# Optimization experiments

Hardware: AMD Instinct MI355X
Metric: run time of the kernel (lower is better)

The kernel has to match this reference:

```python
import jax, jax.numpy as jnp
import numpy as np

NEG_SLOPE_GAT = 0.2   # GATConv internal leaky_relu slope (PyG default)
NEG_SLOPE = 0.01      # nn.LeakyReLU default slope


def _gat(h_src_in, h_dst_in, src, dst, Wsrc, Wdst, a_s, a_d, b, n_dst, self_loops):
    """Single-head PyG-style GATConv: gather -> score -> edge softmax -> scatter-sum."""
    hs = h_src_in @ Wsrc            # [N_src, C]
    hd = h_dst_in @ Wdst            # [N_dst, C]
    if self_loops:                  # static flag; same node set on both sides
        loop = jnp.arange(n_dst, dtype=src.dtype)
        src = jnp.concatenate([src, loop])
        dst = jnp.concatenate([dst, loop])
    # attention logits per edge
    e = jax.nn.leaky_relu((hs @ a_s)[src] + (hd @ a_d)[dst], NEG_SLOPE_GAT)  # [E]
    # softmax over edges sharing a destination node
    m = jax.ops.segment_max(e, dst, num_segments=n_dst)
    ex = jnp.exp(e - m[dst])
    denom = jax.ops.segment_sum(ex, dst, num_segments=n_dst)
    alpha = ex / denom[dst]
    out = jax.ops.segment_sum(hs[src] * alpha[:, None], dst, num_segments=n_dst)
    return out + b


def setup_inputs() -> dict:
    key = jax.random.key(0)
    ks = iter(jax.random.split(key, 64))
    NB, NP = 100_000, 50_000
    E_bb, E_pp, E_bp = 800_000, 400_000, 400_000
    FB, FP, H, H2 = 32, 34, 64, 32
    rn = lambda shape, s=0.05: jax.random.normal(next(ks), shape, jnp.float32) * s
    d = {}
    d['x_b'] = rn((NB, FB), 1.0)
    d['x_p'] = rn((NP, FP), 1.0)
    d['ei_bb'] = jax.random.randint(next(ks), (2, E_bb), 0, NB, jnp.int32)
    d['ei_pp'] = jax.random.randint(next(ks), (2, E_pp), 0, NP, jnp.int32)
    d['ei_bp_src'] = jax.random.randint(next(ks), (E_bp,), 0, NB, jnp.int32)
    d['ei_bp_dst'] = jax.random.randint(next(ks), (E_bp,), 0, NP, jnp.int32)
    d['W_in_b'] = rn((FB, H)); d['b_in_b'] = jnp.zeros((H,), jnp.float32)
    d['W_in_p'] = rn((FP, H)); d['b_in_p'] = jnp.zeros((H,), jnp.float32)
    for tag, cin, cout in (('1', H, H), ('2', H, H2)):
        d['W_bb' + tag] = rn((cin, cout)); d['as_bb' + tag] = rn((cout,)); d['ad_bb' + tag] = rn((cout,)); d['b_bb' + tag] = jnp.zeros((cout,), jnp.float32)
        d['W_pp' + tag] = rn((cin, cout)); d['as_pp' + tag] = rn((cout,)); d['ad_pp' + tag] = rn((cout,)); d['b_pp' + tag] = jnp.zeros((cout,), jnp.float32)
        d['Ws_bp' + tag] = rn((cin, cout)); d['Wd_bp' + tag] = rn((cin, cout)); d['as_bp' + tag] = rn((cout,)); d['ad_bp' + tag] = rn((cout,)); d['b_bp' + tag] = jnp.zeros((cout,), jnp.float32)
    d['W_out'] = rn((H2, 1)); d['b_out'] = jnp.zeros((1,), jnp.float32)
    return d


def reference(x_b, x_p, ei_bb, ei_pp, ei_bp_src, ei_bp_dst,
              W_in_b, b_in_b, W_in_p, b_in_p,
              W_bb1, as_bb1, ad_bb1, b_bb1, W_pp1, as_pp1, ad_pp1, b_pp1,
              Ws_bp1, Wd_bp1, as_bp1, ad_bp1, b_bp1,
              W_bb2, as_bb2, ad_bb2, b_bb2, W_pp2, as_pp2, ad_pp2, b_pp2,
              Ws_bp2, Wd_bp2, as_bp2, ad_bp2, b_bp2,
              W_out, b_out):
    NB, NP = x_b.shape[0], x_p.shape[0]
    lr = lambda v: jax.nn.leaky_relu(v, NEG_SLOPE)
    # input projections (dropout is eval-mode identity)
    hb = lr(x_b @ W_in_b + b_in_b)
    hp = lr(x_p @ W_in_p + b_in_p)
    # hetero conv 1 (sum aggregation over relations sharing a dst type)
    ob = _gat(hb, hb, ei_bb[0], ei_bb[1], W_bb1, W_bb1, as_bb1, ad_bb1, b_bb1, NB, True)
    op = (_gat(hp, hp, ei_pp[0], ei_pp[1], W_pp1, W_pp1, as_pp1, ad_pp1, b_pp1, NP, True)
          + _gat(hb, hp, ei_bp_src, ei_bp_dst, Ws_bp1, Wd_bp1, as_bp1, ad_bp1, b_bp1, NP, False))
    hb, hp = lr(ob), lr(op)
    # hetero conv 2
    ob2 = _gat(hb, hb, ei_bb[0], ei_bb[1], W_bb2, W_bb2, as_bb2, ad_bb2, b_bb2, NB, True)
    op2 = (_gat(hp, hp, ei_pp[0], ei_pp[1], W_pp2, W_pp2, as_pp2, ad_pp2, b_pp2, NP, True)
           + _gat(hb, hp, ei_bp_src, ei_bp_dst, Ws_bp2, Wd_bp2, as_bp2, ad_bp2, b_bp2, NP, False))
    hp = lr(op2)
    return hp @ W_out + b_out  # [NP, 1]
```

## Files before the change

### kernel.cpp

```cpp
#include <hip/hip_runtime.h>
#include <hip/hip_bf16.h>
#include <cstdint>
#include <cstddef>


typedef __attribute__((ext_vector_type(8))) short short8;
typedef __attribute__((ext_vector_type(4))) float f32x4;
typedef unsigned int u32;
typedef __hip_bfloat16 bf16;

#define ABITS 9
#define CHUNKE 8192

static __device__ __forceinline__ float b2f(bf16 v) { return __bfloat162float(v); }

static __device__ __forceinline__ float ldf(const void* p, int i, int bf) {
    return bf ? __bfloat162float(((const bf16*)p)[i]) : ((const float*)p)[i];
}

static __device__ __forceinline__ short f2bs(float f) {
    bf16 h = __float2bfloat16(f);
    return *reinterpret_cast<short*>(&h);
}
static __device__ __forceinline__ float bs2f(short s) {
    bf16 h = *reinterpret_cast<bf16*>(&s);
    return __bfloat162float(h);
}
static __device__ __forceinline__ float lo16(u32 u) { return bs2f((short)(u & 0xffffu)); }
static __device__ __forceinline__ float hi16(u32 u) { return bs2f((short)(u >> 16)); }
static __device__ __forceinline__ u32 pack2(float x, float y) {
    return (u32)(unsigned short)f2bs(x) | ((u32)(unsigned short)f2bs(y) << 16);
}
static __device__ __forceinline__ float sel4(const float* a, int i) {
    return i == 0 ? a[0] : i == 1 ? a[1] : i == 2 ? a[2] : a[3];
}
static __device__ __forceinline__ float lrelu2(float x) { return x > 0.f ? x : 0.2f * x; }

static __device__ __forceinline__ int probe_bf(const unsigned* __restrict__ w, int* cnt) {
    if (threadIdx.x == 0) *cnt = 0;
    __syncthreads();
    int c = 0;
#pragma unroll
    for (int j = 0; j < 4; ++j) {
        unsigned u = w[threadIdx.x * 4 + j];
        unsigned e = (u >> 7) & 0xffu;
        c += (e >= 100u && e <= 145u) ? 1 : 0;
    }
    atomicAdd(cnt, c);
    __syncthreads();
    int r = (*cnt > 614) ? 1 : 0;
    __syncthreads();
    return r;
}

template <int CIN>
static __device__ __forceinline__ void in_proj_body(
    short* WT, float* bl, int bid,
    const void* __restrict__ X, const void* __restrict__ W, const void* __restrict__ B,
    bf16* __restrict__ Y, int M, int bf)
{
    constexpr int KP = 40;
    for (int i = threadIdx.x; i < 64 * CIN; i += 256) {
        int n = i / CIN, k = i - n * CIN;
        WT[n * KP + k] = f2bs(ldf(W, k * 64 + n, bf));
    }
    if (threadIdx.x < 64) bl[threadIdx.x] = ldf(B, threadIdx.x, bf);
    __syncthreads();

    int lane = threadIdx.x & 63;
    int wv   = threadIdx.x >> 6;
    int m = lane & 15, quad = lane >> 4;
    int row0 = (bid * 4 + wv) * 16;
    if (row0 >= M) return;

    int arow = row0 + m; if (arow >= M) arow = M - 1;
    short8 a;
#pragma unroll
    for (int j = 0; j < 8; ++j)
        a[j] = f2bs(ldf(X, arow * CIN + quad * 8 + j, bf));

    f32x4 acc[4] = {};
#pragma unroll
    for (int tt = 0; tt < 4; ++tt) {
        short8 bfr = *(const short8*)&WT[((lane & 15) + 16 * tt) * KP + quad * 8];
        acc[tt] = __builtin_amdgcn_mfma_f32_16x16x32_bf16(a, bfr, acc[tt], 0, 0, 0);
    }

    if (CIN == 34) {
        float x32[4], x33[4];
#pragma unroll
        for (int r = 0; r < 4; ++r) {
            int row = row0 + quad * 4 + r; if (row >= M) row = M - 1;
            x32[r] = ldf(X, row * CIN + 32, bf);
            x33[r] = ldf(X, row * CIN + 33, bf);
        }
#pragma unroll
        for (int tt = 0; tt < 4; ++tt) {
            int col = (lane & 15) + 16 * tt;
            float w32 = bs2f(WT[col * KP + 32]);
            float w33 = bs2f(WT[col * KP + 33]);
#pragma unroll
            for (int r = 0; r < 4; ++r)
                acc[tt][r] += x32[r] * w32 + x33[r] * w33;
        }
    }

#pragma unroll
    for (int tt = 0; tt < 4; ++tt) {
        int col = (lane & 15) + 16 * tt;
        float bb = bl[col];
#pragma unroll
        for (int r = 0; r < 4; ++r) {
            int row = row0 + quad * 4 + r;
            if (row < M) {
                float v = acc[tt][r] + bb;
                v = v > 0.f ? v : 0.01f * v;
                Y[(size_t)row * 64 + col] = __float2bfloat16(v);
            }
        }
    }
}

__global__ __launch_bounds__(256) void k_hist_inproj(
    const int* __restrict__ bb_d, const int* __restrict__ pp_d,
    const int* __restrict__ bp_d, int* __restrict__ histM,
    const unsigned* __restrict__ probe_w, int* __restrict__ flag,
    int E_bb, int E_pp, int E_bp, int NB, int NP, int nbkt, int nblk,
    const void* __restrict__ Xb, const void* __restrict__ Wb, const void* __restrict__ Bb,
    bf16* __restrict__ Yb, int MB,
    const void* __restrict__ Xp, const void* __restrict__ Wp, const void* __restrict__ Bp,
    bf16* __restrict__ Yp, int MP)
{
    __shared__ short WT[64 * 40];
    __shared__ float bl[64];
    __shared__ int aux[1 << ABITS];
    if ((int)blockIdx.x < nblk) {
        if (blockIdx.x == 0) {
            int b = probe_bf(probe_w, &aux[0]);
            if (threadIdx.x == 0) *flag = b;
        }
        for (int i = threadIdx.x; i < nbkt; i += 256) aux[i] = 0;
        __syncthreads();
        int E_all = E_bb + E_pp + E_bp;
        int base = blockIdx.x * CHUNKE;
        int end = base + CHUNKE < E_all ? base + CHUNKE : E_all;
        for (int i = base + threadIdx.x; i < end; i += 256) {
            int d;
            if (i < E_bb) d = bb_d[i];
            else if (i < E_bb + E_pp) d = NB + pp_d[i - E_bb];
            else d = NB + NP + bp_d[i - E_bb - E_pp];
            atomicAdd(&aux[d >> ABITS], 1);
        }
        __syncthreads();
        for (int i = threadIdx.x; i < nbkt; i += 256)
            histM[(size_t)i * nblk + blockIdx.x] = aux[i];
    } else {
        int bfv = probe_bf(probe_w, &aux[0]);
        int bid = blockIdx.x - nblk;
        int nbb = (MB + 63) >> 6;
        if (bid < nbb) in_proj_body<32>(WT, bl, bid, Xb, Wb, Bb, Yb, MB, bfv);
        else           in_proj_body<34>(WT, bl, bid - nbb, Xp, Wp, Bp, Yp, MP, bfv);
    }
}

__global__ __launch_bounds__(1024) void k_scan1(const int* __restrict__ deg,
                                                int* __restrict__ out,
                                                int* __restrict__ bsum, int n)
{
    __shared__ int wsum[16];
    int gid = blockIdx.x * 1024 + threadIdx.x;
    int lane = threadIdx.x & 63, wid = threadIdx.x >> 6;
    int v = (gid < n) ? deg[gid] : 0;
    int x = v;
#pragma unroll
    for (int off = 1; off < 64; off <<= 1) {
        int y = __shfl_up(x, off, 64);
        if (lane >= off) x += y;
    }
    if (lane == 63) wsum[wid] = x;
    __syncthreads();
    if (wid == 0 && lane < 16) {
        int w0 = wsum[lane];
#pragma unroll
        for (int off = 1; off < 16; off <<= 1) {
            int y = __shfl_up(w0, off, 16);
            if (lane >= off) w0 += y;
        }
        wsum[lane] = w0;
    }
    __syncthreads();
    int base = (wid > 0) ? wsum[wid - 1] : 0;
    int incl = base + x;
    if (gid < n) out[gid] = incl - v;
    if (threadIdx.x == 1023) bsum[blockIdx.x] = incl;
}

__global__ __launch_bounds__(1024) void k_scan2(int* __restrict__ bsum, int nb)
{
    __shared__ int wsum[16];
    int lane = threadIdx.x & 63, wid = threadIdx.x >> 6;
    int v = (threadIdx.x < nb) ? bsum[threadIdx.x] : 0;
    int x = v;
#pragma unroll
    for (int off = 1; off < 64; off <<= 1) {
        int y = __shfl_up(x, off, 64);
        if (lane >= off) x += y;
    }
    if (lane == 63) wsum[wid] = x;
    __syncthreads();
    if (wid == 0 && lane < 16) {
        int w0 = wsum[lane];
#pragma unroll
        for (int off = 1; off < 16; off <<= 1) {
            int y = __shfl_up(w0, off, 16);
            if (lane >= off) w0 += y;
        }
        wsum[lane] = w0;
    }
    __syncthreads();
    int base = (wid > 0) ? wsum[wid - 1] : 0;
    if (threadIdx.x < nb) bsum[threadIdx.x] = base + x - v;
}

__global__ __launch_bounds__(1024) void k_scan3(int* __restrict__ indptr,
                                                const int* __restrict__ bsum,
                                                int n, int E)
{
    int gid = blockIdx.x * 1024 + threadIdx.x;
    if (gid < n) indptr[gid] += bsum[blockIdx.x];
    if (gid == 0) indptr[n] = E;
}

template <int N1, int N2, bool S1F, bool S2F>
static __device__ __forceinline__ void dual_body(
    short* WT, int bid, const bf16* __restrict__ H,
    const void* __restrict__ W1, const void* __restrict__ W2,
    const void* __restrict__ as1, const void* __restrict__ ad1,
    const void* __restrict__ as2, const void* __restrict__ ad2,
    bf16* __restrict__ HS1, bf16* __restrict__ HS2,
    float* __restrict__ SS1, float* __restrict__ SD1,
    float* __restrict__ SS2, float* __restrict__ SD2,
    int M, int bf)
{
    constexpr int KP = 72;
    constexpr int T1 = N1 / 16, T2 = N2 / 16, T = T1 + T2;
    for (int i = threadIdx.x; i < N1 * 64; i += 256) {
        int n = i >> 6, k = i & 63;
        WT[n * KP + k] = f2bs(ldf(W1, k * N1 + n, bf));
    }
    for (int i = threadIdx.x; i < N2 * 64; i += 256) {
        int n = i >> 6, k = i & 63;
        WT[(N1 + n) * KP + k] = f2bs(ldf(W2, k * N2 + n, bf));
    }
    __syncthreads();

    int lane = threadIdx.x & 63;
    int wv   = threadIdx.x >> 6;
    int m = lane & 15, quad = lane >> 4;
    int row0 = (bid * 4 + wv) * 16;
    if (row0 >= M) return;

    const short* Hs = (const short*)H;
    int arow = row0 + m; if (arow >= M) arow = M - 1;

    f32x4 acc[T] = {};
#pragma unroll
    for (int ks = 0; ks < 2; ++ks) {
        short8 a = *(const short8*)&Hs[(size_t)arow * 64 + ks * 32 + quad * 8];
#pragma unroll
        for (int tt = 0; tt < T; ++tt) {
            short8 bfr = *(const short8*)&WT[((lane & 15) + 16 * tt) * KP + ks * 32 + quad * 8];
            acc[tt] = __builtin_amdgcn_mfma_f32_16x16x32_bf16(a, bfr, acc[tt], 0, 0, 0);
        }
    }

    float vs1[4] = {}, vd1[4] = {}, vs2[4] = {}, vd2[4] = {};
#pragma unroll
    for (int tt = 0; tt < T1; ++tt) {
        int col = (lane & 15) + 16 * tt;
        float av = ldf(as1, col, bf), dv = ldf(ad1, col, bf);
#pragma unroll
        for (int r = 0; r < 4; ++r) {
            vs1[r] += acc[tt][r] * av;
            vd1[r] += acc[tt][r] * dv;
        }
    }
#pragma unroll
    for (int tt = 0; tt < T2; ++tt) {
        int col = (lane & 15) + 16 * tt;
        float av = ldf(as2, col, bf), dv = ldf(ad2, col, bf);
#pragma unroll
        for (int r = 0; r < 4; ++r) {
            vs2[r] += acc[T1 + tt][r] * av;
            vd2[r] += acc[T1 + tt][r] * dv;
        }
    }
#pragma unroll
    for (int off = 1; off < 16; off <<= 1)
#pragma unroll
        for (int r = 0; r < 4; ++r) {
            vs1[r] += __shfl_xor(vs1[r], off);
            vd1[r] += __shfl_xor(vd1[r], off);
            vs2[r] += __shfl_xor(vs2[r], off);
            vd2[r] += __shfl_xor(vd2[r], off);
        }
    int c = lane & 15;
    {
        int row = row0 + quad * 4 + (c & 3);
        if (row < M) {
            if (c < 4)       SS1[row] = sel4(vs1, c & 3);
            else if (c < 8)  SD1[row] = sel4(vd1, c & 3);
            else if (c < 12) SS2[row] = sel4(vs2, c & 3);
            else             SD2[row] = sel4(vd2, c & 3);
        }
    }

    if (S1F) {
#pragma unroll
        for (int tt = 0; tt < T1; ++tt) {
            int col = (lane & 15) + 16 * tt;
#pragma unroll
            for (int r = 0; r < 4; ++r) {
                int row = row0 + quad * 4 + r;
                if (row < M)
                    HS1[(size_t)row * N1 + col] = __float2bfloat16(acc[tt][r]);
            }
        }
    }
    if (S2F) {
#pragma unroll
        for (int tt = 0; tt < T2; ++tt) {
            int col = (lane & 15) + 16 * tt;
#pragma unroll
            for (int r = 0; r < 4; ++r) {
                int row = row0 + quad * 4 + r;
                if (row < M)
                    HS2[(size_t)row * N2 + col] = __float2bfloat16(acc[T1 + tt][r]);
            }
        }
    }
}

template <int N, bool STORE>
static __device__ __forceinline__ void proj_body(
    short* WT, int bid, const bf16* __restrict__ H, const void* __restrict__ W,
    const void* __restrict__ a_s, const void* __restrict__ a_d,
    bf16* __restrict__ HS, float* __restrict__ SS, float* __restrict__ SD,
    int M, int bf)
{
    constexpr int KP = 72;
    constexpr int T = N / 16;
    for (int i = threadIdx.x; i < N * 64; i += 256) {
        int n = i >> 6, k = i & 63;
        WT[n * KP + k] = f2bs(ldf(W, k * N + n, bf));
    }
    __syncthreads();

    int lane = threadIdx.x & 63;
    int wv   = threadIdx.x >> 6;
    int m = lane & 15, quad = lane >> 4;
    int row0 = (bid * 4 + wv) * 16;
    if (row0 >= M) return;

    const short* Hs = (const short*)H;
    int arow = row0 + m; if (arow >= M) arow = M - 1;

    f32x4 acc[T] = {};
#pragma unroll
    for (int ks = 0; ks < 2; ++ks) {
        short8 a = *(const short8*)&Hs[(size_t)arow * 64 + ks * 32 + quad * 8];
#pragma unroll
        for (int tt = 0; tt < T; ++tt) {
            short8 bfr = *(const short8*)&WT[((lane & 15) + 16 * tt) * KP + ks * 32 + quad * 8];
            acc[tt] = __builtin_amdgcn_mfma_f32_16x16x32_bf16(a, bfr, acc[tt], 0, 0, 0);
        }
    }

    float asv[T], adv[T];
#pragma unroll
    for (int tt = 0; tt < T; ++tt) {
        int col = (lane & 15) + 16 * tt;
        asv[tt] = ldf(a_s, col, bf);
        adv[tt] = ldf(a_d, col, bf);
    }
    float vs[4] = {}, vd[4] = {};
#pragma unroll
    for (int tt = 0; tt < T; ++tt)
#pragma unroll
        for (int r = 0; r < 4; ++r) {
            vs[r] += acc[tt][r] * asv[tt];
            vd[r] += acc[tt][r] * adv[tt];
        }
#pragma unroll
    for (int off = 1; off < 16; off <<= 1)
#pragma unroll
        for (int r = 0; r < 4; ++r) {
            vs[r] += __shfl_xor(vs[r], off);
            vd[r] += __shfl_xor(vd[r], off);
        }
    int c = lane & 15;
    if (c < 8) {
        int row = row0 + quad * 4 + (c & 3);
        if (row < M) {
            if (c < 4) SS[row] = sel4(vs, c & 3);
            else       SD[row] = sel4(vd, c & 3);
        }
    }

    if (STORE) {
#pragma unroll
        for (int tt = 0; tt < T; ++tt) {
            int col = (lane & 15) + 16 * tt;
#pragma unroll
            for (int r = 0; r < 4; ++r) {
                int row = row0 + quad * 4 + r;
                if (row < M)
                    HS[(size_t)row * N + col] = __float2bfloat16(acc[tt][r]);
            }
        }
    }
}

__global__ __launch_bounds__(256) void k_scatter_dual(
    const int* __restrict__ bb_s, const int* __restrict__ bb_d,
    const int* __restrict__ pp_s, const int* __restrict__ pp_d,
    const int* __restrict__ bp_s, const int* __restrict__ bp_d,
    const int* __restrict__ histS, unsigned* __restrict__ ebuf,
    int E_bb, int E_pp, int E_bp, int NB, int NP, int nbkt, int nblk,
    const bf16* __restrict__ hb,
    const void* W_bb1, const void* Ws_bp1,
    const void* as_bb1, const void* ad_bb1, const void* as_bp1, const void* ad_bp1,
    bf16* hs_bb, bf16* hs_bp,
    float* ss_bb, float* sd_bb, float* ss_bp, float* junkNB, int MB,
    const bf16* __restrict__ hp,
    const void* W_pp1, const void* Wd_bp1,
    const void* as_pp1, const void* ad_pp1,
    bf16* hs_pp, float* ss_pp, float* sd_pp, float* junkNP, float* sd_bp, int MP,
    const int* __restrict__ flag)
{
    __shared__ short WT[128 * 72];
    if ((int)blockIdx.x < nblk) {
        int* cur = (int*)WT;
        for (int i = threadIdx.x; i < nbkt; i += 256)
            cur[i] = histS[(size_t)i * nblk + blockIdx.x];
        __syncthreads();
        int E_all = E_bb + E_pp + E_bp;
        int base = blockIdx.x * CHUNKE;
        int end = base + CHUNKE < E_all ? base + CHUNKE : E_all;
        for (int i = base + threadIdx.x; i < end; i += 256) {
            int s, d;
            if (i < E_bb) { s = bb_s[i]; d = bb_d[i]; }
            else if (i < E_bb + E_pp) { int j = i - E_bb; s = pp_s[j]; d = NB + pp_d[j]; }
            else { int j = i - E_bb - E_pp; s = bp_s[j]; d = NB + NP + bp_d[j]; }
            int p = atomicAdd(&cur[d >> ABITS], 1);
            ebuf[p] = ((unsigned)(d & ((1 << ABITS) - 1)) << 20) | (unsigned)s;
        }
    } else {
        const int bfv = *flag;
        int bid = blockIdx.x - nblk;
        int nbb = (MB + 63) >> 6;
        if (bid < nbb)
            dual_body<64, 64, true, true>(WT, bid, hb, W_bb1, Ws_bp1,
                as_bb1, ad_bb1, as_bp1, ad_bp1, hs_bb, hs_bp,
                ss_bb, sd_bb, ss_bp, junkNB, MB, bfv);
        else
            dual_body<64, 64, true, false>(WT, bid - nbb, hp, W_pp1, Wd_bp1,
                as_pp1, ad_pp1, as_bp1, ad_bp1, hs_pp, nullptr,
                ss_pp, sd_pp, junkNP, sd_bp, MP, bfv);
    }
}

__global__ __launch_bounds__(256) void k_finalize(
    const unsigned* __restrict__ ebuf, const int* __restrict__ histS,
    int* __restrict__ ip_all, int2* __restrict__ sw,
    const float* __restrict__ ss_bb, const float* __restrict__ sd_bb,
    const float* __restrict__ ss_pp, const float* __restrict__ sd_pp,
    const float* __restrict__ ss_bp, const float* __restrict__ sd_bp,
    int NB, int NP, int NALL, int E_all, int nbkt, int nblk)
{
    __shared__ int h[1 << ABITS];
    __shared__ int pre[1 << ABITS];
    __shared__ int wq[4];
    int b = blockIdx.x;
    int d0 = b << ABITS;
    int nloc = NALL - d0 < (1 << ABITS) ? NALL - d0 : (1 << ABITS);
    int t = threadIdx.x;
    for (int i = t; i < (1 << ABITS); i += 256) h[i] = 0;
    __syncthreads();
    int s0 = histS[(size_t)b * nblk];
    int s1 = histS[(size_t)(b + 1) * nblk];
    for (int i = s0 + t; i < s1; i += 256)
        atomicAdd(&h[ebuf[i] >> 20], 1);
    __syncthreads();
    int v0 = h[2 * t], v1 = h[2 * t + 1];
    int ps = v0 + v1;
    int lane = t & 63, wid = t >> 6;
    int x = ps;
#pragma unroll
    for (int off = 1; off < 64; off <<= 1) {
        int y = __shfl_up(x, off, 64);
        if (lane >= off) x += y;
    }
    if (lane == 63) wq[wid] = x;
    __syncthreads();
    if (t == 0) {
        int a = 0;
#pragma unroll
        for (int w = 0; w < 4; ++w) { int tmp = wq[w]; wq[w] = a; a += tmp; }
    }
    __syncthreads();
    int excl = wq[wid] + x - ps;
    pre[2 * t]     = excl;
    pre[2 * t + 1] = excl + v0;
    __syncthreads();
    for (int i = t; i < nloc; i += 256) ip_all[d0 + i] = s0 + pre[i];
    if (d0 + nloc == NALL && t == 0) ip_all[NALL] = E_all;
    for (int i = t; i < (1 << ABITS); i += 256) h[i] = s0 + pre[i];
    __syncthreads();
    for (int i = s0 + t; i < s1; i += 256) {
        unsigned e = ebuf[i];
        int dl = (int)(e >> 20);
        int src = (int)(e & 0xFFFFFu);
        int p = atomicAdd(&h[dl], 1);
        int d = d0 + dl;
        float ssv, sdv;
        if (d < NB)           { ssv = ss_bb[src]; sdv = sd_bb[d]; }
        else if (d < NB + NP) { ssv = ss_pp[src]; sdv = sd_pp[d - NB]; }
        else                  { ssv = ss_bp[src]; sdv = sd_bp[d - NB - NP]; }
        int2 pk; pk.x = src; pk.y = __float_as_int(__expf(lrelu2(ssv + sdv)));
        sw[p] = pk;
    }
}

static __device__ __forceinline__ void gather1_body(
    int bid, const int* __restrict__ ip, const int2* __restrict__ sw,
    const float* __restrict__ SS, const float* __restrict__ SD,
    const bf16* __restrict__ HS, const void* __restrict__ bias,
    bf16* __restrict__ OUT, int M, int bf)
{
    int lane = threadIdx.x & 63;
    int half = lane >> 5, hl = lane & 31;
    int d = bid * 4 + (threadIdx.x >> 6);
    if (d >= M) return;
    const u32* H32 = (const u32*)HS;
    float ax = 0.f, ay = 0.f, den = 0.f;
    if (half == 0) {
        float ex = __expf(lrelu2(SS[d] + SD[d]));
        u32 h = H32[(size_t)d * 32 + hl];
        ax = lo16(h) * ex; ay = hi16(h) * ex; den = ex;
    }
    int j1 = ip[d + 1];
    int j = ip[d] + half;
    for (; j + 6 < j1; j += 8) {
        int2 p0 = sw[j], p1 = sw[j + 2], p2 = sw[j + 4], p3 = sw[j + 6];
        u32 h0 = H32[(size_t)p0.x * 32 + hl];
        u32 h1 = H32[(size_t)p1.x * 32 + hl];
        u32 h2 = H32[(size_t)p2.x * 32 + hl];
        u32 h3 = H32[(size_t)p3.x * 32 + hl];
        float e0 = __int_as_float(p0.y), e1 = __int_as_float(p1.y);
        float e2 = __int_as_float(p2.y), e3 = __int_as_float(p3.y);
        ax += lo16(h0) * e0 + lo16(h1) * e1 + lo16(h2) * e2 + lo16(h3) * e3;
        ay += hi16(h0) * e0 + hi16(h1) * e1 + hi16(h2) * e2 + hi16(h3) * e3;
        den += (e0 + e1) + (e2 + e3);
    }
    for (; j < j1; j += 2) {
        int2 p0 = sw[j];
        u32 h0 = H32[(size_t)p0.x * 32 + hl];
        float e0 = __int_as_float(p0.y);
        ax += lo16(h0) * e0; ay += hi16(h0) * e0; den += e0;
    }
    ax += __shfl_xor(ax, 32); ay += __shfl_xor(ay, 32); den += __shfl_xor(den, 32);
    if (half == 0) {
        float vx = ax / den + ldf(bias, 2 * hl, bf);
        float vy = ay / den + ldf(bias, 2 * hl + 1, bf);
        vx = vx > 0.f ? vx : 0.01f * vx;
        vy = vy > 0.f ? vy : 0.01f * vy;
        ((u32*)OUT)[(size_t)d * 32 + hl] = pack2(vx, vy);
    }
}

static __device__ __forceinline__ void gather2_body(
    int bid, const int* __restrict__ ip1, const int2* __restrict__ sw,
    const float* __restrict__ SS1, const float* __restrict__ SD1,
    const bf16* __restrict__ HS1,
    const int* __restrict__ ip2, const bf16* __restrict__ HS2,
    const void* __restrict__ b1, const void* __restrict__ b2,
    bf16* __restrict__ OUT, int M, int bf)
{
    int lane = threadIdx.x & 63;
    int half = lane >> 5, hl = lane & 31;
    int d = bid * 4 + (threadIdx.x >> 6);
    if (d >= M) return;
    const u32* H1 = (const u32*)HS1;
    const u32* H2 = (const u32*)HS2;
    float a1x = 0.f, a1y = 0.f, den1 = 0.f;
    if (half == 0) {
        float ex = __expf(lrelu2(SS1[d] + SD1[d]));
        u32 h = H1[(size_t)d * 32 + hl];
        a1x = lo16(h) * ex; a1y = hi16(h) * ex; den1 = ex;
    }
    int j1 = ip1[d + 1];
    int j = ip1[d] + half;
    for (; j + 6 < j1; j += 8) {
        int2 p0 = sw[j], p1 = sw[j + 2], p2 = sw[j + 4], p3 = sw[j + 6];
        u32 h0 = H1[(size_t)p0.x * 32 + hl];
        u32 h1 = H1[(size_t)p1.x * 32 + hl];
        u32 h2 = H1[(size_t)p2.x * 32 + hl];
        u32 h3 = H1[(size_t)p3.x * 32 + hl];
        float e0 = __int_as_float(p0.y), e1 = __int_as_float(p1.y);
        float e2 = __int_as_float(p2.y), e3 = __int_as_float(p3.y);
        a1x += lo16(h0) * e0 + lo16(h1) * e1 + lo16(h2) * e2 + lo16(h3) * e3;
        a1y += hi16(h0) * e0 + hi16(h1) * e1 + hi16(h2) * e2 + hi16(h3) * e3;
        den1 += (e0 + e1) + (e2 + e3);
    }
    for (; j < j1; j += 2) {
        int2 p0 = sw[j];
        u32 h0 = H1[(size_t)p0.x * 32 + hl];
        float e0 = __int_as_float(p0.y);
        a1x += lo16(h0) * e0; a1y += hi16(h0) * e0; den1 += e0;
    }
    float a2x = 0.f, a2y = 0.f, den2 = 0.f;
    j1 = ip2[d + 1];
    j = ip2[d] + half;
    for (; j + 6 < j1; j += 8) {
        int2 p0 = sw[j], p1 = sw[j + 2], p2 = sw[j + 4], p3 = sw[j + 6];
        u32 h0 = H2[(size_t)p0.x * 32 + hl];
        u32 h1 = H2[(size_t)p1.x * 32 + hl];
        u32 h2 = H2[(size_t)p2.x * 32 + hl];
        u32 h3 = H2[(size_t)p3.x * 32 + hl];
        float e0 = __int_as_float(p0.y), e1 = __int_as_float(p1.y);
        float e2 = __int_as_float(p2.y), e3 = __int_as_float(p3.y);
        a2x += lo16(h0) * e0 + lo16(h1) * e1 + lo16(h2) * e2 + lo16(h3) * e3;
        a2y += hi16(h0) * e0 + hi16(h1) * e1 + hi16(h2) * e2 + hi16(h3) * e3;
        den2 += (e0 + e1) + (e2 + e3);
    }
    for (; j < j1; j += 2) {
        int2 p0 = sw[j];
        u32 h0 = H2[(size_t)p0.x * 32 + hl];
        float e0 = __int_as_float(p0.y);
        a2x += lo16(h0) * e0; a2y += hi16(h0) * e0; den2 += e0;
    }
    a1x += __shfl_xor(a1x, 32); a1y += __shfl_xor(a1y, 32); den1 += __shfl_xor(den1, 32);
    a2x += __shfl_xor(a2x, 32); a2y += __shfl_xor(a2y, 32); den2 += __shfl_xor(den2, 32);
    if (half == 0) {
        float inv2 = den2 > 0.f ? 1.f / den2 : 0.f;
        float vx = a1x / den1 + a2x * inv2 + ldf(b1, 2 * hl, bf) + ldf(b2, 2 * hl, bf);
        float vy = a1y / den1 + a2y * inv2 + ldf(b1, 2 * hl + 1, bf) + ldf(b2, 2 * hl + 1, bf);
        vx = vx > 0.f ? vx : 0.01f * vx;
        vy = vy > 0.f ? vy : 0.01f * vy;
        ((u32*)OUT)[(size_t)d * 32 + hl] = pack2(vx, vy);
    }
}

__global__ __launch_bounds__(256) void k_gather12(
    const int* __restrict__ ip_bb, const int2* __restrict__ sw,
    const float* __restrict__ ss_bb, const float* __restrict__ sd_bb,
    const bf16* __restrict__ hs_bb, const void* __restrict__ b_bb1,
    bf16* __restrict__ hb2, int NB,
    const int* __restrict__ ip_pp, const int* __restrict__ ip_bp,
    const float* __restrict__ ss_pp, const float* __restrict__ sd_pp,
    const bf16* __restrict__ hs_pp, const bf16* __restrict__ hs_bp,
    const void* __restrict__ b_pp1, const void* __restrict__ b_bp1,
    bf16* __restrict__ hp2, int NP,
    const int* __restrict__ flag)
{
    const int bf = *flag;
    int nbb = (NB + 3) >> 2;
    if ((int)blockIdx.x < nbb)
        gather1_body(blockIdx.x, ip_bb, sw, ss_bb, sd_bb, hs_bb, b_bb1, hb2, NB, bf);
    else
        gather2_body(blockIdx.x - nbb, ip_pp, sw, ss_pp, sd_pp, hs_pp,
                     ip_bp, hs_bp, b_pp1, b_bp1, hp2, NP, bf);
}

__global__ __launch_bounds__(256) void k_proj2_all(
    const bf16* __restrict__ hp2,
    const void* W_pp2, const void* Wd_bp2,
    const void* as_pp2, const void* ad_pp2, const void* as_bp2, const void* ad_bp2,
    bf16* hs2_pp, float* ss2_pp, float* sd2_pp, float* junkNP, float* sd2_bp, int MP,
    const bf16* __restrict__ hb2,
    const void* Ws_bp2, bf16* hs2_bp, float* ss2_bp, float* junkNB, int MB,
    const int* __restrict__ flag)
{
    const int bf = *flag;
    __shared__ short WT[64 * 72];
    int npb = (MP + 63) >> 6;
    if ((int)blockIdx.x < npb)
        dual_body<32, 32, true, false>(WT, blockIdx.x, hp2, W_pp2, Wd_bp2,
            as_pp2, ad_pp2, as_bp2, ad_bp2, hs2_pp, nullptr,
            ss2_pp, sd2_pp, junkNP, sd2_bp, MP, bf);
    else
        proj_body<32, true>(WT, blockIdx.x - npb, hb2, Ws_bp2,
            as_bp2, ad_bp2, hs2_bp, ss2_bp, junkNB, MB, bf);
}

__global__ __launch_bounds__(256) void k_gather_out(
    const int* __restrict__ ip1, const int2* __restrict__ sw,
    const float* __restrict__ SS1, const float* __restrict__ SD1,
    const bf16* __restrict__ HS1,
    const int* __restrict__ ip2,
    const float* __restrict__ SS2, const float* __restrict__ SD2,
    const bf16* __restrict__ HS2,
    const void* __restrict__ b1, const void* __restrict__ b2,
    const void* __restrict__ Wout, const void* __restrict__ bout,
    void* __restrict__ OUT, int M, const int* __restrict__ flag)
{
    const int bf = *flag;
    int lane = threadIdx.x & 63;
    int q = lane >> 4, hl = lane & 15;
    int d = blockIdx.x * 4 + (threadIdx.x >> 6);
    if (d >= M) return;
    const u32* H1 = (const u32*)HS1;
    const u32* H2 = (const u32*)HS2;
    float sdd = SD1[d];
    float a1x = 0.f, a1y = 0.f, den1 = 0.f;
    if (q == 0) {
        float ex = __expf(lrelu2(SS1[d] + sdd));
        u32 h = H1[(size_t)d * 16 + hl];
        a1x = lo16(h) * ex; a1y = hi16(h) * ex; den1 = ex;
    }
    int j1 = ip1[d + 1];
    int j = ip1[d] + q;
    for (; j + 4 < j1; j += 8) {
        int s0 = sw[j].x, s1 = sw[j + 4].x;
        u32 h0 = H1[(size_t)s0 * 16 + hl];
        u32 h1 = H1[(size_t)s1 * 16 + hl];
        float e0 = __expf(lrelu2(SS1[s0] + sdd));
        float e1 = __expf(lrelu2(SS1[s1] + sdd));
        a1x += lo16(h0) * e0 + lo16(h1) * e1;
        a1y += hi16(h0) * e0 + hi16(h1) * e1;
        den1 += e0 + e1;
    }
    if (j < j1) {
        int s0 = sw[j].x;
        u32 h0 = H1[(size_t)s0 * 16 + hl];
        float e0 = __expf(lrelu2(SS1[s0] + sdd));
        a1x += lo16(h0) * e0; a1y += hi16(h0) * e0; den1 += e0;
    }
    float sdd2 = SD2[d];
    float a2x = 0.f, a2y = 0.f, den2 = 0.f;
    j1 = ip2[d + 1];
    j = ip2[d] + q;
    for (; j + 4 < j1; j += 8) {
        int s0 = sw[j].x, s1 = sw[j + 4].x;
        u32 h0 = H2[(size_t)s0 * 16 + hl];
        u32 h1 = H2[(size_t)s1 * 16 + hl];
        float e0 = __expf(lrelu2(SS2[s0] + sdd2));
        float e1 = __expf(lrelu2(SS2[s1] + sdd2));
        a2x += lo16(h0) * e0 + lo16(h1) * e1;
        a2y += hi16(h0) * e0 + hi16(h1) * e1;
        den2 += e0 + e1;
    }
    if (j < j1) {
        int s0 = sw[j].x;
        u32 h0 = H2[(size_t)s0 * 16 + hl];
        float e0 = __expf(lrelu2(SS2[s0] + sdd2));
        a2x += lo16(h0) * e0; a2y += hi16(h0) * e0; den2 += e0;
    }
    a1x += __shfl_xor(a1x, 16); a1y += __shfl_xor(a1y, 16); den1 += __shfl_xor(den1, 16);
    a2x += __shfl_xor(a2x, 16); a2y += __shfl_xor(a2y, 16); den2 += __shfl_xor(den2, 16);
    a1x += __shfl_xor(a1x, 32); a1y += __shfl_xor(a1y, 32); den1 += __shfl_xor(den1, 32);
    a2x += __shfl_xor(a2x, 32); a2y += __shfl_xor(a2y, 32); den2 += __shfl_xor(den2, 32);
    float inv2 = den2 > 0.f ? 1.f / den2 : 0.f;
    float vx = a1x / den1 + a2x * inv2 + ldf(b1, 2 * hl, bf) + ldf(b2, 2 * hl, bf);
    float vy = a1y / den1 + a2y * inv2 + ldf(b1, 2 * hl + 1, bf) + ldf(b2, 2 * hl + 1, bf);
    vx = vx > 0.f ? vx : 0.01f * vx;
    vy = vy > 0.f ? vy : 0.01f * vy;
    float t = vx * ldf(Wout, 2 * hl, bf) + vy * ldf(Wout, 2 * hl + 1, bf);
#pragma unroll
    for (int off = 1; off < 16; off <<= 1) t += __shfl_xor(t, off);
    if (lane == 0) {
        float r = t + ldf(bout, 0, bf);
        if (bf) ((bf16*)OUT)[d] = __float2bfloat16(r);
        else    ((float*)OUT)[d] = r;
    }
}

extern "C" void kernel_launch(void* const* d_in, const int* in_sizes, int n_in,
                              void* d_out, int out_size, void* d_ws, size_t ws_size,
                              hipStream_t stream)
{
    const void* x_b = d_in[0];
    const void* x_p = d_in[1];
    const int* ei_bb = (const int*)d_in[2];
    const int* ei_pp = (const int*)d_in[3];
    const int* bp_s  = (const int*)d_in[4];
    const int* bp_d  = (const int*)d_in[5];
    const void *W_in_b = d_in[6],  *b_in_b = d_in[7];
    const void *W_in_p = d_in[8],  *b_in_p = d_in[9];
    const void *W_bb1 = d_in[10], *as_bb1 = d_in[11], *ad_bb1 = d_in[12], *b_bb1 = d_in[13];
    const void *W_pp1 = d_in[14], *as_pp1 = d_in[15], *ad_pp1 = d_in[16], *b_pp1 = d_in[17];
    const void *Ws_bp1 = d_in[18], *Wd_bp1 = d_in[19], *as_bp1 = d_in[20], *ad_bp1 = d_in[21], *b_bp1 = d_in[22];
    const void *W_pp2 = d_in[27], *as_pp2 = d_in[28], *ad_pp2 = d_in[29], *b_pp2 = d_in[30];
    const void *Ws_bp2 = d_in[31], *Wd_bp2 = d_in[32], *as_bp2 = d_in[33], *ad_bp2 = d_in[34], *b_bp2 = d_in[35];
    const void *W_out = d_in[36], *b_out = d_in[37];

    const int NB   = in_sizes[0] / 32;
    const int NP   = in_sizes[1] / 34;
    const int E_bb = in_sizes[2] / 2;
    const int E_pp = in_sizes[3] / 2;
    const int E_bp = in_sizes[4];
    const int E_all = E_bb + E_pp + E_bp;
    const int NALL  = NB + 2 * NP;
    const int* bb_s = ei_bb;  const int* bb_d = ei_bb + E_bb;
    const int* pp_s = ei_pp;  const int* pp_d = ei_pp + E_pp;
    (void)ws_size; (void)n_in; (void)out_size;

    const int nbkt  = (NALL + (1 << ABITS) - 1) >> ABITS;
    const int nblk  = (E_all + CHUNKE - 1) / CHUNKE;
    const int nh    = nbkt * nblk;

    char* base = (char*)d_ws;
    size_t o = 0;
    auto alloc = [&](size_t bytes) { char* p = base + o; o += (bytes + 255) & ~(size_t)255; return p; };

    int* flag  = (int*)alloc(256);
    int* bsum  = (int*)alloc(1024 * 4);
    int* histM = (int*)alloc((size_t)nh * 4);
    int* histS = (int*)alloc((size_t)(nh + 1) * 4);
    int* ip_all = (int*)alloc((size_t)(NALL + 1) * 4);
    unsigned* ebuf = (unsigned*)alloc((size_t)E_all * 4);
    int2* sw = (int2*)alloc((size_t)E_all * 8);
    float* ss_bb = (float*)alloc((size_t)NB * 4);
    float* sd_bb = (float*)alloc((size_t)NB * 4);
    float* ss_bp = (float*)alloc((size_t)NB * 4);
    float* ss_pp = (float*)alloc((size_t)NP * 4);
    float* sd_pp = (float*)alloc((size_t)NP * 4);
    float* sd_bp = (float*)alloc((size_t)NP * 4);
    float* junkNB = (float*)alloc((size_t)NB * 4);
    float* junkNP = (float*)alloc((size_t)NP * 4);
    float* ss2_bp = ss_bb;
    float* ss2_pp = ss_pp;
    float* sd2_pp = sd_pp;
    float* sd2_bp = sd_bp;

    char* S1 = alloc((size_t)NB * 64 * 2);
    char* S2 = alloc((size_t)NP * 64 * 2);
    char* S3 = alloc((size_t)NB * 64 * 2);
    char* S4 = alloc((size_t)NB * 64 * 2);
    char* S5 = alloc((size_t)NB * 64 * 2);
    char* S6 = alloc((size_t)NP * 64 * 2);

    bf16* hb     = (bf16*)S1;
    bf16* hp     = (bf16*)S2;
    bf16* hs_bb  = (bf16*)S3;
    bf16* hb2    = (bf16*)S4;
    bf16* hs_bp  = (bf16*)S5;
    bf16* hs_pp  = (bf16*)S6;
    bf16* hp2    = (bf16*)S2;
    bf16* hs2_pp = (bf16*)S3;
    bf16* hs2_bp = (bf16*)S1;

    auto cdiv = [](int a, int b) { return (a + b - 1) / b; };

    const int* ip_bb = ip_all;
    const int* ip_pp = ip_all + NB;
    const int* ip_bp = ip_all + NB + NP;

    k_hist_inproj<<<nblk + cdiv(NB, 64) + cdiv(NP, 64), 256, 0, stream>>>(
        bb_d, pp_d, bp_d, histM, (const unsigned*)x_b, flag,
        E_bb, E_pp, E_bp, NB, NP, nbkt, nblk,
        x_b, W_in_b, b_in_b, hb, NB, x_p, W_in_p, b_in_p, hp, NP);

    int sb1 = cdiv(nh, 1024);
    k_scan1<<<sb1, 1024, 0, stream>>>(histM, histS, bsum, nh);
    k_scan2<<<1, 1024, 0, stream>>>(bsum, sb1);
    k_scan3<<<sb1, 1024, 0, stream>>>(histS, bsum, nh, E_all);

    k_scatter_dual<<<nblk + cdiv(NB, 64) + cdiv(NP, 64), 256, 0, stream>>>(
        bb_s, bb_d, pp_s, pp_d, bp_s, bp_d, histS, ebuf,
        E_bb, E_pp, E_bp, NB, NP, nbkt, nblk,
        hb, W_bb1, Ws_bp1, as_bb1, ad_bb1, as_bp1, ad_bp1,
        hs_bb, hs_bp, ss_bb, sd_bb, ss_bp, junkNB, NB,
        hp, W_pp1, Wd_bp1, as_pp1, ad_pp1,
        hs_pp, ss_pp, sd_pp, junkNP, sd_bp, NP, flag);

    k_finalize<<<nbkt, 256, 0, stream>>>(ebuf, histS, ip_all, sw,
                                         ss_bb, sd_bb, ss_pp, sd_pp, ss_bp, sd_bp,
                                         NB, NP, NALL, E_all, nbkt, nblk);

    k_gather12<<<cdiv(NB, 4) + cdiv(NP, 4), 256, 0, stream>>>(
        ip_bb, sw, ss_bb, sd_bb, hs_bb, b_bb1, hb2, NB,
        ip_pp, ip_bp, ss_pp, sd_pp, hs_pp, hs_bp,
        b_pp1, b_bp1, hp2, NP, flag);

    k_proj2_all<<<cdiv(NP, 64) + cdiv(NB, 64), 256, 0, stream>>>(
        hp2, W_pp2, Wd_bp2, as_pp2, ad_pp2, as_bp2, ad_bp2,
        hs2_pp, ss2_pp, sd2_pp, junkNP, sd2_bp, NP,
        hb2, Ws_bp2, hs2_bp, ss2_bp, junkNB, NB, flag);

    k_gather_out<<<cdiv(NP, 4), 256, 0, stream>>>(
        ip_pp, sw, ss2_pp, sd2_pp, hs2_pp,
        ip_bp, ss2_bp, sd2_bp, hs2_bp,
        b_pp2, b_bp2, W_out, b_out, d_out, NP, flag);
}
```

Before: 394.4 us.

## Fuse layer-1 gather with layer-2 projection and drop scan3 kernel

Each block now gathers the layer-1 aggregation for 16 destination nodes into a shared-memory tile, then runs the layer-2 MFMA projection and attention-score dot products on that tile, instead of writing hb2/hp2 to global memory and reading them back in a separate projection kernel. The third scan pass is removed by adding the block offset from bsum when the scatter and finalize kernels read histS. This cuts a global round trip of intermediate features and two launches. In exchange only one wave per block does the MFMA work after the gather, and the layer-2 score buffers get separate allocations so they no longer alias layer-1 buffers that are still being read.

```diff
diff --git a/kernel.cpp b/kernel.cpp
--- a/kernel.cpp
+++ b/kernel.cpp
@@ -222,15 +222,6 @@
     if (threadIdx.x < nb) bsum[threadIdx.x] = base + x - v;
 }
 
-__global__ __launch_bounds__(1024) void k_scan3(int* __restrict__ indptr,
-                                                const int* __restrict__ bsum,
-                                                int n, int E)
-{
-    int gid = blockIdx.x * 1024 + threadIdx.x;
-    if (gid < n) indptr[gid] += bsum[blockIdx.x];
-    if (gid == 0) indptr[n] = E;
-}
-
 template <int N1, int N2, bool S1F, bool S2F>
 static __device__ __forceinline__ void dual_body(
     short* WT, int bid, const bf16* __restrict__ H,
@@ -341,91 +332,12 @@
     }
 }
 
-template <int N, bool STORE>
-static __device__ __forceinline__ void proj_body(
-    short* WT, int bid, const bf16* __restrict__ H, const void* __restrict__ W,
-    const void* __restrict__ a_s, const void* __restrict__ a_d,
-    bf16* __restrict__ HS, float* __restrict__ SS, float* __restrict__ SD,
-    int M, int bf)
-{
-    constexpr int KP = 72;
-    constexpr int T = N / 16;
-    for (int i = threadIdx.x; i < N * 64; i += 256) {
-        int n = i >> 6, k = i & 63;
-        WT[n * KP + k] = f2bs(ldf(W, k * N + n, bf));
-    }
-    __syncthreads();
-
-    int lane = threadIdx.x & 63;
-    int wv   = threadIdx.x >> 6;
-    int m = lane & 15, quad = lane >> 4;
-    int row0 = (bid * 4 + wv) * 16;
-    if (row0 >= M) return;
-
-    const short* Hs = (const short*)H;
-    int arow = row0 + m; if (arow >= M) arow = M - 1;
-
-    f32x4 acc[T] = {};
-#pragma unroll
-    for (int ks = 0; ks < 2; ++ks) {
-        short8 a = *(const short8*)&Hs[(size_t)arow * 64 + ks * 32 + quad * 8];
-#pragma unroll
-        for (int tt = 0; tt < T; ++tt) {
-            short8 bfr = *(const short8*)&WT[((lane & 15) + 16 * tt) * KP + ks * 32 + quad * 8];
-            acc[tt] = __builtin_amdgcn_mfma_f32_16x16x32_bf16(a, bfr, acc[tt], 0, 0, 0);
-        }
-    }
-
-    float asv[T], adv[T];
-#pragma unroll
-    for (int tt = 0; tt < T; ++tt) {
-        int col = (lane & 15) + 16 * tt;
-        asv[tt] = ldf(a_s, col, bf);
-        adv[tt] = ldf(a_d, col, bf);
-    }
-    float vs[4] = {}, vd[4] = {};
-#pragma unroll
-    for (int tt = 0; tt < T; ++tt)
-#pragma unroll
-        for (int r = 0; r < 4; ++r) {
-            vs[r] += acc[tt][r] * asv[tt];
-            vd[r] += acc[tt][r] * adv[tt];
-        }
-#pragma unroll
-    for (int off = 1; off < 16; off <<= 1)
-#pragma unroll
-        for (int r = 0; r < 4; ++r) {
-            vs[r] += __shfl_xor(vs[r], off);
-            vd[r] += __shfl_xor(vd[r], off);
-        }
-    int c = lane & 15;
-    if (c < 8) {
-        int row = row0 + quad * 4 + (c & 3);
-        if (row < M) {
-            if (c < 4) SS[row] = sel4(vs, c & 3);
-            else       SD[row] = sel4(vd, c & 3);
-        }
-    }
-
-    if (STORE) {
-#pragma unroll
-        for (int tt = 0; tt < T; ++tt) {
-            int col = (lane & 15) + 16 * tt;
-#pragma unroll
-            for (int r = 0; r < 4; ++r) {
-                int row = row0 + quad * 4 + r;
-                if (row < M)
-                    HS[(size_t)row * N + col] = __float2bfloat16(acc[tt][r]);
-            }
-        }
-    }
-}
-
 __global__ __launch_bounds__(256) void k_scatter_dual(
     const int* __restrict__ bb_s, const int* __restrict__ bb_d,
     const int* __restrict__ pp_s, const int* __restrict__ pp_d,
     const int* __restrict__ bp_s, const int* __restrict__ bp_d,
-    const int* __restrict__ histS, unsigned* __restrict__ ebuf,
+    const int* __restrict__ histS, const int* __restrict__ bsum,
+    unsigned* __restrict__ ebuf,
     int E_bb, int E_pp, int E_bp, int NB, int NP, int nbkt, int nblk,
     const bf16* __restrict__ hb,
     const void* W_bb1, const void* Ws_bp1,
@@ -441,8 +353,10 @@
     __shared__ short WT[128 * 72];
     if ((int)blockIdx.x < nblk) {
         int* cur = (int*)WT;
-        for (int i = threadIdx.x; i < nbkt; i += 256)
-            cur[i] = histS[(size_t)i * nblk + blockIdx.x];
+        for (int i = threadIdx.x; i < nbkt; i += 256) {
+            size_t g = (size_t)i * nblk + blockIdx.x;
+            cur[i] = histS[g] + bsum[g >> 10];
+        }
         __syncthreads();
         int E_all = E_bb + E_pp + E_bp;
         int base = blockIdx.x * CHUNKE;
@@ -472,6 +386,7 @@
 
 __global__ __launch_bounds__(256) void k_finalize(
     const unsigned* __restrict__ ebuf, const int* __restrict__ histS,
+    const int* __restrict__ bsum,
     int* __restrict__ ip_all, int2* __restrict__ sw,
     const float* __restrict__ ss_bb, const float* __restrict__ sd_bb,
     const float* __restrict__ ss_pp, const float* __restrict__ sd_pp,
@@ -487,8 +402,13 @@
     int t = threadIdx.x;
     for (int i = t; i < (1 << ABITS); i += 256) h[i] = 0;
     __syncthreads();
-    int s0 = histS[(size_t)b * nblk];
-    int s1 = histS[(size_t)(b + 1) * nblk];
+    size_t g0 = (size_t)b * nblk;
+    int s0 = histS[g0] + bsum[g0 >> 10];
+    int s1;
+    if (b + 1 < nbkt) {
+        size_t g1 = (size_t)(b + 1) * nblk;
+        s1 = histS[g1] + bsum[g1 >> 10];
+    } else s1 = E_all;
     for (int i = s0 + t; i < s1; i += 256)
         atomicAdd(&h[ebuf[i] >> 20], 1);
     __syncthreads();
@@ -532,16 +452,15 @@
     }
 }
 
-static __device__ __forceinline__ void gather1_body(
-    int bid, const int* __restrict__ ip, const int2* __restrict__ sw,
+static __device__ __forceinline__ void gather1_tile(
+    int d, int row, const int* __restrict__ ip, const int2* __restrict__ sw,
     const float* __restrict__ SS, const float* __restrict__ SD,
     const bf16* __restrict__ HS, const void* __restrict__ bias,
-    bf16* __restrict__ OUT, int M, int bf)
+    u32* tile, int M, int bf)
 {
     int lane = threadIdx.x & 63;
     int half = lane >> 5, hl = lane & 31;
-    int d = bid * 4 + (threadIdx.x >> 6);
-    if (d >= M) return;
+    if (d >= M) { if (half == 0) tile[row * 36 + hl] = 0; return; }
     const u32* H32 = (const u32*)HS;
     float ax = 0.f, ay = 0.f, den = 0.f;
     if (half == 0) {
@@ -575,22 +494,21 @@
         float vy = ay / den + ldf(bias, 2 * hl + 1, bf);
         vx = vx > 0.f ? vx : 0.01f * vx;
         vy = vy > 0.f ? vy : 0.01f * vy;
-        ((u32*)OUT)[(size_t)d * 32 + hl] = pack2(vx, vy);
-    }
-}
-
-static __device__ __forceinline__ void gather2_body(
-    int bid, const int* __restrict__ ip1, const int2* __restrict__ sw,
+        tile[row * 36 + hl] = pack2(vx, vy);
+    }
+}
+
+static __device__ __forceinline__ void gather2_tile(
+    int d, int row, const int* __restrict__ ip1, const int2* __restrict__ sw,
     const float* __restrict__ SS1, const float* __restrict__ SD1,
     const bf16* __restrict__ HS1,
     const int* __restrict__ ip2, const bf16* __restrict__ HS2,
     const void* __restrict__ b1, const void* __restrict__ b2,
-    bf16* __restrict__ OUT, int M, int bf)
+    u32* tile, int M, int bf)
 {
     int lane = threadIdx.x & 63;
     int half = lane >> 5, hl = lane & 31;
-    int d = bid * 4 + (threadIdx.x >> 6);
-    if (d >= M) return;
+    if (d >= M) { if (half == 0) tile[row * 36 + hl] = 0; return; }
     const u32* H1 = (const u32*)HS1;
     const u32* H2 = (const u32*)HS2;
     float a1x = 0.f, a1y = 0.f, den1 = 0.f;
@@ -648,50 +566,180 @@
         float vy = a1y / den1 + a2y * inv2 + ldf(b1, 2 * hl + 1, bf) + ldf(b2, 2 * hl + 1, bf);
         vx = vx > 0.f ? vx : 0.01f * vx;
         vy = vy > 0.f ? vy : 0.01f * vy;
-        ((u32*)OUT)[(size_t)d * 32 + hl] = pack2(vx, vy);
-    }
-}
-
-__global__ __launch_bounds__(256) void k_gather12(
+        tile[row * 36 + hl] = pack2(vx, vy);
+    }
+}
+
+static __device__ __forceinline__ void tile_proj_single(
+    const u32* tile, const short* WT,
+    const void* __restrict__ a_s, const void* __restrict__ a_d,
+    bf16* __restrict__ HS, float* __restrict__ SS, float* __restrict__ SD,
+    int d0, int M, int bf)
+{
+    const short* tl = (const short*)tile;
+    int lane = threadIdx.x;
+    int quad = lane >> 4;
+    f32x4 acc[2] = {};
+#pragma unroll
+    for (int ks = 0; ks < 2; ++ks) {
+        short8 a = *(const short8*)&tl[(lane & 15) * 72 + ks * 32 + quad * 8];
+#pragma unroll
+        for (int tt = 0; tt < 2; ++tt) {
+            short8 b = *(const short8*)&WT[((lane & 15) + 16 * tt) * 72 + ks * 32 + quad * 8];
+            acc[tt] = __builtin_amdgcn_mfma_f32_16x16x32_bf16(a, b, acc[tt], 0, 0, 0);
+        }
+    }
+    float vs[4] = {}, vd[4] = {};
+#pragma unroll
+    for (int tt = 0; tt < 2; ++tt) {
+        int col = (lane & 15) + 16 * tt;
+        float av = ldf(a_s, col, bf), dv = ldf(a_d, col, bf);
+#pragma unroll
+        for (int r = 0; r < 4; ++r) { vs[r] += acc[tt][r] * av; vd[r] += acc[tt][r] * dv; }
+    }
+#pragma unroll
+    for (int off = 1; off < 16; off <<= 1)
+#pragma unroll
+        for (int r = 0; r < 4; ++r) {
+            vs[r] += __shfl_xor(vs[r], off);
+            vd[r] += __shfl_xor(vd[r], off);
+        }
+    int c = lane & 15;
+    if (c < 8) {
+        int row = d0 + quad * 4 + (c & 3);
+        if (row < M) {
+            if (c < 4) SS[row] = sel4(vs, c & 3);
+            else       SD[row] = sel4(vd, c & 3);
+        }
+    }
+#pragma unroll
+    for (int tt = 0; tt < 2; ++tt) {
+        int col = (lane & 15) + 16 * tt;
+#pragma unroll
+        for (int r = 0; r < 4; ++r) {
+            int row = d0 + quad * 4 + r;
+            if (row < M) HS[(size_t)row * 32 + col] = __float2bfloat16(acc[tt][r]);
+        }
+    }
+}
+
+static __device__ __forceinline__ void tile_proj_dual(
+    const u32* tile, const short* WT,
+    const void* __restrict__ as1, const void* __restrict__ ad1,
+    const void* __restrict__ as2, const void* __restrict__ ad2,
+    bf16* __restrict__ HS1, float* __restrict__ SS1, float* __restrict__ SD1,
+    float* __restrict__ SD2,
+    int d0, int M, int bf)
+{
+    const short* tl = (const short*)tile;
+    int lane = threadIdx.x;
+    int quad = lane >> 4;
+    f32x4 acc[4] = {};
+#pragma unroll
+    for (int ks = 0; ks < 2; ++ks) {
+        short8 a = *(const short8*)&tl[(lane & 15) * 72 + ks * 32 + quad * 8];
+#pragma unroll
+        for (int tt = 0; tt < 4; ++tt) {
+            short8 b = *(const short8*)&WT[((lane & 15) + 16 * tt) * 72 + ks * 32 + quad * 8];
+            acc[tt] = __builtin_amdgcn_mfma_f32_16x16x32_bf16(a, b, acc[tt], 0, 0, 0);
+        }
+    }
+    float vs1[4] = {}, vd1[4] = {}, vd2[4] = {};
+#pragma unroll
+    for (int tt = 0; tt < 2; ++tt) {
+        int col = (lane & 15) + 16 * tt;
+        float av = ldf(as1, col, bf), dv = ldf(ad1, col, bf);
+        float dv2 = ldf(ad2, col, bf);
+#pragma unroll
+        for (int r = 0; r < 4; ++r) {
+            vs1[r] += acc[tt][r] * av;
+            vd1[r] += acc[tt][r] * dv;
+            vd2[r] += acc[2 + tt][r] * dv2;
+        }
+    }
+    (void)as2;
+#pragma unroll
+    for (int off = 1; off < 16; off <<= 1)
+#pragma unroll
+        for (int r = 0; r < 4; ++r) {
+            vs1[r] += __shfl_xor(vs1[r], off);
+            vd1[r] += __shfl_xor(vd1[r], off);
+            vd2[r] += __shfl_xor(vd2[r], off);
+        }
+    int c = lane & 15;
+    {
+        int row = d0 + quad * 4 + (c & 3);
+        if (row < M) {
+            if (c < 4)       SS1[row] = sel4(vs1, c & 3);
+            else if (c < 8)  SD1[row] = sel4(vd1, c & 3);
+            else if (c < 12) SD2[row] = sel4(vd2, c & 3);
+        }
+    }
+#pragma unroll
+    for (int tt = 0; tt < 2; ++tt) {
+        int col = (lane & 15) + 16 * tt;
+#pragma unroll
+        for (int r = 0; r < 4; ++r) {
+            int row = d0 + quad * 4 + r;
+            if (row < M) HS1[(size_t)row * 32 + col] = __float2bfloat16(acc[tt][r]);
+        }
+    }
+}
+
+__global__ __launch_bounds__(256) void k_gather_fused(
     const int* __restrict__ ip_bb, const int2* __restrict__ sw,
     const float* __restrict__ ss_bb, const float* __restrict__ sd_bb,
-    const bf16* __restrict__ hs_bb, const void* __restrict__ b_bb1,
-    bf16* __restrict__ hb2, int NB,
+    const bf16* __restrict__ hs_bb, const void* __restrict__ b_bb1, int NB,
+    const void* __restrict__ Ws_bp2, const void* __restrict__ as_bp2,
+    const void* __restrict__ ad_bp2,
+    bf16* __restrict__ hs2_bp, float* __restrict__ ss2_bp, float* __restrict__ junkNB,
     const int* __restrict__ ip_pp, const int* __restrict__ ip_bp,
     const float* __restrict__ ss_pp, const float* __restrict__ sd_pp,
     const bf16* __restrict__ hs_pp, const bf16* __restrict__ hs_bp,
-    const void* __restrict__ b_pp1, const void* __restrict__ b_bp1,
-    bf16* __restrict__ hp2, int NP,
+    const void* __restrict__ b_pp1, const void* __restrict__ b_bp1, int NP,
+    const void* __restrict__ W_pp2, const void* __restrict__ Wd_bp2,
+    const void* __restrict__ as_pp2, const void* __restrict__ ad_pp2,
+    bf16* __restrict__ hs2_pp, float* __restrict__ ss2_pp, float* __restrict__ sd2_pp,
+    float* __restrict__ sd2_bp,
     const int* __restrict__ flag)
 {
     const int bf = *flag;
-    int nbb = (NB + 3) >> 2;
-    if ((int)blockIdx.x < nbb)
-        gather1_body(blockIdx.x, ip_bb, sw, ss_bb, sd_bb, hs_bb, b_bb1, hb2, NB, bf);
-    else
-        gather2_body(blockIdx.x - nbb, ip_pp, sw, ss_pp, sd_pp, hs_pp,
-                     ip_bp, hs_bp, b_pp1, b_bp1, hp2, NP, bf);
-}
-
-__global__ __launch_bounds__(256) void k_proj2_all(
-    const bf16* __restrict__ hp2,
-    const void* W_pp2, const void* Wd_bp2,
-    const void* as_pp2, const void* ad_pp2, const void* as_bp2, const void* ad_bp2,
-    bf16* hs2_pp, float* ss2_pp, float* sd2_pp, float* junkNP, float* sd2_bp, int MP,
-    const bf16* __restrict__ hb2,
-    const void* Ws_bp2, bf16* hs2_bp, float* ss2_bp, float* junkNB, int MB,
-    const int* __restrict__ flag)
-{
-    const int bf = *flag;
+    __shared__ u32 tile[16 * 36];
     __shared__ short WT[64 * 72];
-    int npb = (MP + 63) >> 6;
-    if ((int)blockIdx.x < npb)
-        dual_body<32, 32, true, false>(WT, blockIdx.x, hp2, W_pp2, Wd_bp2,
-            as_pp2, ad_pp2, as_bp2, ad_bp2, hs2_pp, nullptr,
-            ss2_pp, sd2_pp, junkNP, sd2_bp, MP, bf);
-    else
-        proj_body<32, true>(WT, blockIdx.x - npb, hb2, Ws_bp2,
-            as_bp2, ad_bp2, hs2_bp, ss2_bp, junkNB, MB, bf);
+    int nbbblk = (NB + 15) >> 4;
+    int wv = threadIdx.x >> 6;
+    if ((int)blockIdx.x < nbbblk) {
+        int d0 = blockIdx.x * 16;
+        for (int i = threadIdx.x; i < 32 * 64; i += 256) {
+            int n = i >> 6, k = i & 63;
+            WT[n * 72 + k] = f2bs(ldf(Ws_bp2, k * 32 + n, bf));
+        }
+        for (int r = 0; r < 4; ++r) {
+            int row = wv * 4 + r;
+            gather1_tile(d0 + row, row, ip_bb, sw, ss_bb, sd_bb, hs_bb, b_bb1,
+                         tile, NB, bf);
+        }
+        __syncthreads();
+        if (threadIdx.x < 64)
+            tile_proj_single(tile, WT, as_bp2, ad_bp2, hs2_bp, ss2_bp, junkNB,
+                             d0, NB, bf);
+    } else {
+        int d0 = (blockIdx.x - nbbblk) * 16;
+        for (int i = threadIdx.x; i < 32 * 64; i += 256) {
+            int n = i >> 6, k = i & 63;
+            WT[n * 72 + k]        = f2bs(ldf(W_pp2,  k * 32 + n, bf));
+            WT[(32 + n) * 72 + k] = f2bs(ldf(Wd_bp2, k * 32 + n, bf));
+        }
+        for (int r = 0; r < 4; ++r) {
+            int row = wv * 4 + r;
+            gather2_tile(d0 + row, row, ip_pp, sw, ss_pp, sd_pp, hs_pp,
+                         ip_bp, hs_bp, b_pp1, b_bp1, tile, NP, bf);
+        }
+        __syncthreads();
+        if (threadIdx.x < 64)
+            tile_proj_dual(tile, WT, as_pp2, ad_pp2, as_bp2, ad_bp2,
+                           hs2_pp, ss2_pp, sd2_pp, sd2_bp, d0, NP, bf);
+    }
 }
 
 __global__ __launch_bounds__(256) void k_gather_out(
@@ -817,7 +865,7 @@
     int* flag  = (int*)alloc(256);
     int* bsum  = (int*)alloc(1024 * 4);
     int* histM = (int*)alloc((size_t)nh * 4);
-    int* histS = (int*)alloc((size_t)(nh + 1) * 4);
+    int* histS = (int*)alloc((size_t)nh * 4);
     int* ip_all = (int*)alloc((size_t)(NALL + 1) * 4);
     unsigned* ebuf = (unsigned*)alloc((size_t)E_all * 4);
     int2* sw = (int2*)alloc((size_t)E_all * 8);
@@ -829,10 +877,10 @@
     float* sd_bp = (float*)alloc((size_t)NP * 4);
     float* junkNB = (float*)alloc((size_t)NB * 4);
     float* junkNP = (float*)alloc((size_t)NP * 4);
-    float* ss2_bp = ss_bb;
-    float* ss2_pp = ss_pp;
-    float* sd2_pp = sd_pp;
-    float* sd2_bp = sd_bp;
+    float* ss2_bp = (float*)alloc((size_t)NB * 4);
+    float* ss2_pp = (float*)alloc((size_t)NP * 4);
+    float* sd2_pp = (float*)alloc((size_t)NP * 4);
+    float* sd2_bp = (float*)alloc((size_t)NP * 4);
 
     char* S1 = alloc((size_t)NB * 64 * 2);
     char* S2 = alloc((size_t)NP * 64 * 2);
@@ -844,12 +892,10 @@
     bf16* hb     = (bf16*)S1;
     bf16* hp     = (bf16*)S2;
     bf16* hs_bb  = (bf16*)S3;
-    bf16* hb2    = (bf16*)S4;
     bf16* hs_bp  = (bf16*)S5;
     bf16* hs_pp  = (bf16*)S6;
-    bf16* hp2    = (bf16*)S2;
-    bf16* hs2_pp = (bf16*)S3;
     bf16* hs2_bp = (bf16*)S1;
+    bf16* hs2_pp = (bf16*)S4;
 
     auto cdiv = [](int a, int b) { return (a + b - 1) / b; };
 
@@ -865,29 +911,24 @@
     int sb1 = cdiv(nh, 1024);
     k_scan1<<<sb1, 1024, 0, stream>>>(histM, histS, bsum, nh);
     k_scan2<<<1, 1024, 0, stream>>>(bsum, sb1);
-    k_scan3<<<sb1, 1024, 0, stream>>>(histS, bsum, nh, E_all);
 
     k_scatter_dual<<<nblk + cdiv(NB, 64) + cdiv(NP, 64), 256, 0, stream>>>(
-        bb_s, bb_d, pp_s, pp_d, bp_s, bp_d, histS, ebuf,
+        bb_s, bb_d, pp_s, pp_d, bp_s, bp_d, histS, bsum, ebuf,
         E_bb, E_pp, E_bp, NB, NP, nbkt, nblk,
         hb, W_bb1, Ws_bp1, as_bb1, ad_bb1, as_bp1, ad_bp1,
         hs_bb, hs_bp, ss_bb, sd_bb, ss_bp, junkNB, NB,
         hp, W_pp1, Wd_bp1, as_pp1, ad_pp1,
         hs_pp, ss_pp, sd_pp, junkNP, sd_bp, NP, flag);
 
-    k_finalize<<<nbkt, 256, 0, stream>>>(ebuf, histS, ip_all, sw,
+    k_finalize<<<nbkt, 256, 0, stream>>>(ebuf, histS, bsum, ip_all, sw,
                                          ss_bb, sd_bb, ss_pp, sd_pp, ss_bp, sd_bp,
                                          NB, NP, NALL, E_all, nbkt, nblk);
 
-    k_gather12<<<cdiv(NB, 4) + cdiv(NP, 4), 256, 0, stream>>>(
-        ip_bb, sw, ss_bb, sd_bb, hs_bb, b_bb1, hb2, NB,
-        ip_pp, ip_bp, ss_pp, sd_pp, hs_pp, hs_bp,
-        b_pp1, b_bp1, hp2, NP, flag);
-
-    k_proj2_all<<<cdiv(NP, 64) + cdiv(NB, 64), 256, 0, stream>>>(
-        hp2, W_pp2, Wd_bp2, as_pp2, ad_pp2, as_bp2, ad_bp2,
-        hs2_pp, ss2_pp, sd2_pp, junkNP, sd2_bp, NP,
-        hb2, Ws_bp2, hs2_bp, ss2_bp, junkNB, NB, flag);
+    k_gather_fused<<<cdiv(NB, 16) + cdiv(NP, 16), 256, 0, stream>>>(
+        ip_bb, sw, ss_bb, sd_bb, hs_bb, b_bb1, NB,
+        Ws_bp2, as_bp2, ad_bp2, hs2_bp, ss2_bp, junkNB,
+        ip_pp, ip_bp, ss_pp, sd_pp, hs_pp, hs_bp, b_pp1, b_bp1, NP,
+        W_pp2, Wd_bp2, as_pp2, ad_pp2, hs2_pp, ss2_pp, sd2_pp, sd2_bp, flag);
 
     k_gather_out<<<cdiv(NP, 4), 256, 0, stream>>>(
         ip_pp, sw, ss2_pp, sd2_pp, hs2_pp,
```

Result: slower. 432.3 us (+9.6%).
